# Optimization experiments

Measured on AMD Instinct MI355X. Metric: run time of the kernel, lower is better.

## Reference

```python
import jax, jax.numpy as jnp
import numpy as np
import math

B, T, C = 1, 2048, 2048
H, KVH = 32, 8
D = C // H  # 64
EPS = 1e-5
ROPE_THETA = 10000.0


def rmsnorm(x, w):
    # RMSNorm over last axis (head_dim), matches flax RMSNorm applied per-head
    var = jnp.mean(jnp.square(x), axis=-1, keepdims=True)
    return x * jax.lax.rsqrt(var + EPS) * w


def apply_rope(x, cos, sin):
    # x: [B, T, h, D]; cos/sin: [T, D//2]
    xr = x.reshape(*x.shape[:-1], D // 2, 2)
    x0, x1 = xr[..., 0], xr[..., 1]
    c = cos.reshape(1, T, 1, D // 2)
    s = sin.reshape(1, T, 1, D // 2)
    o0 = x0 * c - x1 * s
    o1 = x0 * s + x1 * c
    return jnp.stack([o0, o1], axis=-1).reshape(x.shape)


def setup_inputs() -> dict:
    key = jax.random.key(0)
    ks = jax.random.split(key, 12)
    x = jax.random.normal(ks[0], (B, T, C), jnp.float32)
    # RoPE tables
    inv_freq = 1.0 / (ROPE_THETA ** (np.arange(0, D, 2, dtype=np.float32) / D))
    angles = np.arange(T, dtype=np.float32)[:, None] * inv_freq[None, :]  # [T, D//2]
    freqs_cos = jnp.asarray(np.cos(angles))
    freqs_sin = jnp.asarray(np.sin(angles))
    # causal additive mask [1,1,T,T]
    causal = np.triu(np.full((T, T), -1e9, dtype=np.float32), k=1)
    mask = jnp.asarray(causal)[None, None]
    sc = lambda f: 1.0 / math.sqrt(f)
    return {
        "x": x,
        "freqs_cos": freqs_cos,
        "freqs_sin": freqs_sin,
        "mask": mask,
        "wq_k": jax.random.normal(ks[1], (C, H * D), jnp.float32) * sc(C),
        "wq_b": jnp.zeros((H * D,), jnp.float32),
        "wk_k": jax.random.normal(ks[2], (C, KVH * D), jnp.float32) * sc(C),
        "wk_b": jnp.zeros((KVH * D,), jnp.float32),
        "wv_k": jax.random.normal(ks[3], (C, KVH * D), jnp.float32) * sc(C),
        "wv_b": jnp.zeros((KVH * D,), jnp.float32),
        "wo_k": jax.random.normal(ks[4], (H * D, C), jnp.float32) * sc(H * D),
        "wo_b": jnp.zeros((C,), jnp.float32),
        "qn_w": jnp.ones((D,), jnp.float32),
        "kn_w": jnp.ones((D,), jnp.float32),
    }


def reference(x, freqs_cos, freqs_sin, mask, wq_k, wq_b, wk_k, wk_b, wv_k, wv_b, wo_k, wo_b, qn_w, kn_w):
    q = (x @ wq_k + wq_b).reshape(B, T, H, D)
    k = (x @ wk_k + wk_b).reshape(B, T, KVH, D)
    v = (x @ wv_k + wv_b).reshape(B, T, KVH, D)
    # QK RMSNorm over head_dim
    q = rmsnorm(q, qn_w)
    k = rmsnorm(k, kn_w)
    # RoPE
    q = apply_rope(q, freqs_cos, freqs_sin)
    k = apply_rope(k, freqs_cos, freqs_sin)
    # GQA repeat kv heads
    rep = H // KVH
    k = jnp.repeat(k, rep, axis=2)
    v = jnp.repeat(v, rep, axis=2)
    # [B, H, T, D]
    q, k, v = (jnp.swapaxes(t, 1, 2) for t in (q, k, v))
    scale = 1.0 / math.sqrt(D)
    scores = jnp.einsum("bhqd,bhkd->bhqk", q, k) * scale + mask
    attn = jax.nn.softmax(scores, axis=-1)
    out = jnp.einsum("bhqk,bhkd->bhqd", attn, v)
    out = jnp.swapaxes(out, 1, 2).reshape(B, T, H * D)
    return out @ wo_k + wo_b
```

## Files before the change

kernel.cpp:

```cpp
#include <hip/hip_runtime.h>
#include <hip/hip_bf16.h>
#include <cstdint>

typedef unsigned short u16;
typedef __attribute__((ext_vector_type(8))) short short8;
typedef __attribute__((ext_vector_type(4))) float f32x4;

__device__ __forceinline__ u16 f2bf(float f) {
  union { float f; uint32_t u; } c; c.f = f;
  return (u16)((c.u + 0x7FFFu + ((c.u >> 16) & 1u)) >> 16);
}

__device__ __forceinline__ uint32_t pack_bf16x2(float a, float b) {
  union { __hip_bfloat162 h; uint32_t u; } c;
  c.h = __float22bfloat162_rn(make_float2(a, b));
  return c.u;
}

__global__ __launch_bounds__(256) void prep_kernel(const float* __restrict__ x,
                                                   u16* __restrict__ xb,
                                                   const float* __restrict__ wq,
                                                   const float* __restrict__ wk,
                                                   const float* __restrict__ wv,
                                                   const float* __restrict__ wo,
                                                   u16* __restrict__ wqkvT,
                                                   u16* __restrict__ woT) {
  int id = blockIdx.x;
  if (id >= 2560) {
    int i = (id - 2560) * 256 + threadIdx.x;
    float4 v = ((const float4*)x)[i];
    ((ushort4*)xb)[i] = make_ushort4(f2bf(v.x), f2bf(v.y), f2bf(v.z), f2bf(v.w));
    return;
  }
  __shared__ float tile[64][65];
  const int K = 2048;
  int bx = id % 80, by = id / 80;
  const float* in; u16* out; int N, nx;
  if (bx < 32)      { in = wq; out = wqkvT;                          N = 2048; nx = bx; }
  else if (bx < 40) { in = wk; out = wqkvT + (size_t)2048 * 2048;    N = 512;  nx = bx - 32; }
  else if (bx < 48) { in = wv; out = wqkvT + (size_t)2560 * 2048;    N = 512;  nx = bx - 40; }
  else              { in = wo; out = woT;                            N = 2048; nx = bx - 48; }
  int n0 = nx * 64, k0 = by * 64;
  int t = threadIdx.x;
  int a = t & 63, b4 = t >> 6;
#pragma unroll
  for (int j = 0; j < 16; ++j) {
    int kk = j * 4 + b4;
    tile[kk][a] = in[(size_t)(k0 + kk) * N + n0 + a];
  }
  __syncthreads();
#pragma unroll
  for (int j = 0; j < 16; ++j) {
    int nn = j * 4 + b4;
    out[(size_t)(n0 + nn) * K + k0 + a] = f2bf(tile[a][nn]);
  }
}

__global__ __launch_bounds__(256, 3) void gemm_qkv(const u16* __restrict__ A,
                                                   const u16* __restrict__ Bt,
                                                   const float* __restrict__ wq_b,
                                                   const float* __restrict__ wk_b,
                                                   const float* __restrict__ wv_b,
                                                   const float* __restrict__ qn_w,
                                                   const float* __restrict__ kn_w,
                                                   const float* __restrict__ fc,
                                                   const float* __restrict__ fs,
                                                   u16* __restrict__ Qg,
                                                   u16* __restrict__ Kg,
                                                   u16* __restrict__ Vgt) {
  const int K = 2048;
  __shared__ alignas(16) u16 As[2][64 * 64];
  __shared__ alignas(16) u16 Bs[2][128 * 64];
  int nwg = gridDim.x;
  int cpx = nwg >> 3;
  int bid = blockIdx.x;
  int swz = (bid & 7) * cpx + (bid >> 3);
  int m0 = (swz & 31) << 6;
  int n0 = (swz >> 5) << 7;
  int tid = threadIdx.x;
  int w = tid >> 6, lane = tid & 63;
  int wr = w >> 1, wc = w & 1;
  int fr = lane & 15, hi = lane >> 4;
  int sw = fr & 7;

  auto STAGE = [&](int buf, int kt) {
#pragma unroll
    for (int i = 0; i < 2; ++i) {
      int chunk = i * 256 + tid;
      int row = chunk >> 3, c = chunk & 7;
      const u16* ga = A + (size_t)(m0 + row) * K + kt + ((c ^ (row & 7)) << 3);
      u16* la = &As[buf][(size_t)(i * 256 + w * 64) * 8];
      __builtin_amdgcn_global_load_lds((const __attribute__((address_space(1))) void*)ga,
                                       (__attribute__((address_space(3))) void*)la, 16, 0, 0);
    }
#pragma unroll
    for (int i = 0; i < 4; ++i) {
      int chunk = i * 256 + tid;
      int row = chunk >> 3, c = chunk & 7;
      const u16* gb = Bt + (size_t)(n0 + row) * K + kt + ((c ^ (row & 7)) << 3);
      u16* lb = &Bs[buf][(size_t)(i * 256 + w * 64) * 8];
      __builtin_amdgcn_global_load_lds((const __attribute__((address_space(1))) void*)gb,
                                       (__attribute__((address_space(3))) void*)lb, 16, 0, 0);
    }
  };

  f32x4 acc[2][4] = {};
  STAGE(0, 0);
  __syncthreads();
  int cur = 0;
  int c0 = (hi ^ sw) << 3, c1 = ((4 + hi) ^ sw) << 3;
  for (int kt = 0; kt < K; kt += 64) {
    if (kt + 64 < K) STAGE(cur ^ 1, kt + 64);
    short8 af[2][2], bf[4][2];
#pragma unroll
    for (int m = 0; m < 2; ++m) {
      int rb = (wr * 32 + m * 16 + fr) * 64;
      af[m][0] = *(const short8*)&As[cur][rb + c0];
      af[m][1] = *(const short8*)&As[cur][rb + c1];
    }
#pragma unroll
    for (int n = 0; n < 4; ++n) {
      int rb = (wc * 64 + n * 16 + fr) * 64;
      bf[n][0] = *(const short8*)&Bs[cur][rb + c0];
      bf[n][1] = *(const short8*)&Bs[cur][rb + c1];
    }
#pragma unroll
    for (int m = 0; m < 2; ++m)
#pragma unroll
      for (int n = 0; n < 4; ++n) {
        acc[m][n] = __builtin_amdgcn_mfma_f32_16x16x32_bf16(af[m][0], bf[n][0], acc[m][n], 0, 0, 0);
        acc[m][n] = __builtin_amdgcn_mfma_f32_16x16x32_bf16(af[m][1], bf[n][1], acc[m][n], 0, 0, 0);
      }
    __syncthreads();
    cur ^= 1;
  }

  int fbase = n0 + wc * 64;
  if (fbase >= 2560) {
    const float* bias = wv_b + (fbase - 2560);
    u16* vt = Vgt + (size_t)(fbase - 2560) * 2048;
    float bv[4];
#pragma unroll
    for (int n = 0; n < 4; ++n) bv[n] = bias[n * 16 + fr];
#pragma unroll
    for (int m = 0; m < 2; ++m)
#pragma unroll
      for (int r = 0; r < 4; ++r) {
        int t = m0 + wr * 32 + m * 16 + hi * 4 + r;
#pragma unroll
        for (int n = 0; n < 4; ++n)
          vt[(size_t)(n * 16 + fr) * 2048 + t] = f2bf(acc[m][n][r] + bv[n]);
      }
    return;
  }
  bool isQ = (fbase < 2048);
  const float* bias = isQ ? wq_b + fbase : wk_b + (fbase - 2048);
  const float* nw   = isQ ? qn_w : kn_w;
  float nscale      = isQ ? 0.18033688f : 1.0f;
  u16* outp = isQ ? Qg + (size_t)(fbase >> 6) * 2048 * 64
                  : Kg + (size_t)((fbase - 2048) >> 6) * 2048 * 64;
  float bv[4], nwv[4];
#pragma unroll
  for (int n = 0; n < 4; ++n) {
    bv[n] = bias[n * 16 + fr];
    nwv[n] = nw[n * 16 + fr] * nscale;
  }
#pragma unroll
  for (int m = 0; m < 2; ++m) {
#pragma unroll
    for (int r = 0; r < 4; ++r) {
      int t = m0 + wr * 32 + m * 16 + hi * 4 + r;
      float v[4];
      float sq = 0.0f;
#pragma unroll
      for (int n = 0; n < 4; ++n) { v[n] = acc[m][n][r] + bv[n]; sq += v[n] * v[n]; }
      sq += __shfl_xor(sq, 1); sq += __shfl_xor(sq, 2);
      sq += __shfl_xor(sq, 4); sq += __shfl_xor(sq, 8);
      float rr = rsqrtf(sq * (1.0f / 64.0f) + 1e-5f);
#pragma unroll
      for (int n = 0; n < 4; ++n) {
        float vn = v[n] * rr * nwv[n];
        float part = __shfl_xor(vn, 1);
        int dh = n * 16 + fr;
        float c = fc[t * 32 + (dh >> 1)];
        float s = fs[t * 32 + (dh >> 1)];
        v[n] = (dh & 1) ? (part * s + vn * c) : (vn * c - part * s);
      }
#pragma unroll
      for (int n = 0; n < 4; ++n)
        outp[(size_t)t * 64 + n * 16 + fr] = f2bf(v[n]);
    }
  }
}

__global__ __launch_bounds__(256, 4) void gemm_bt(const u16* __restrict__ A,
                                                  const u16* __restrict__ Bt,
                                                  float* __restrict__ C,
                                                  const float* __restrict__ bias,
                                                  int M, int N, int K) {
  __shared__ alignas(16) u16 As[2][64 * 64];
  __shared__ alignas(16) u16 Bs[2][64 * 64];
  int mt = M >> 6;
  int nwg = gridDim.x;
  int cpx = nwg >> 3;
  int bid = blockIdx.x;
  int swz = (bid & 7) * cpx + (bid >> 3);
  int m0 = (swz % mt) << 6;
  int n0 = (swz / mt) << 6;
  int tid = threadIdx.x;
  int w = tid >> 6, lane = tid & 63;
  int wr = w >> 1, wc = w & 1;
  int fr = lane & 15, hi = lane >> 4;
  int sw = fr & 7;

  auto STAGE = [&](int buf, int kt) {
#pragma unroll
    for (int i = 0; i < 2; ++i) {
      int chunk = i * 256 + tid;
      int row = chunk >> 3, c = chunk & 7;
      const u16* ga = A + (size_t)(m0 + row) * K + kt + ((c ^ (row & 7)) << 3);
      u16* la = &As[buf][(size_t)(i * 256 + w * 64) * 8];
      __builtin_amdgcn_global_load_lds((const __attribute__((address_space(1))) void*)ga,
                                       (__attribute__((address_space(3))) void*)la, 16, 0, 0);
      const u16* gb = Bt + (size_t)(n0 + row) * K + kt + ((c ^ (row & 7)) << 3);
      u16* lb = &Bs[buf][(size_t)(i * 256 + w * 64) * 8];
      __builtin_amdgcn_global_load_lds((const __attribute__((address_space(1))) void*)gb,
                                       (__attribute__((address_space(3))) void*)lb, 16, 0, 0);
    }
  };

  f32x4 acc[2][2] = {};
  STAGE(0, 0);
  __syncthreads();
  int cur = 0;
  int c0 = (hi ^ sw) << 3, c1 = ((4 + hi) ^ sw) << 3;
  for (int kt = 0; kt < K; kt += 64) {
    if (kt + 64 < K) STAGE(cur ^ 1, kt + 64);
    short8 af[2][2], bf[2][2];
#pragma unroll
    for (int m = 0; m < 2; ++m) {
      int rb = (wr * 32 + m * 16 + fr) * 64;
      af[m][0] = *(const short8*)&As[cur][rb + c0];
      af[m][1] = *(const short8*)&As[cur][rb + c1];
    }
#pragma unroll
    for (int n = 0; n < 2; ++n) {
      int rb = (wc * 32 + n * 16 + fr) * 64;
      bf[n][0] = *(const short8*)&Bs[cur][rb + c0];
      bf[n][1] = *(const short8*)&Bs[cur][rb + c1];
    }
#pragma unroll
    for (int m = 0; m < 2; ++m)
#pragma unroll
      for (int n = 0; n < 2; ++n) {
        acc[m][n] = __builtin_amdgcn_mfma_f32_16x16x32_bf16(af[m][0], bf[n][0], acc[m][n], 0, 0, 0);
        acc[m][n] = __builtin_amdgcn_mfma_f32_16x16x32_bf16(af[m][1], bf[n][1], acc[m][n], 0, 0, 0);
      }
    __syncthreads();
    cur ^= 1;
  }
#pragma unroll
  for (int m = 0; m < 2; ++m) {
#pragma unroll
    for (int n = 0; n < 2; ++n) {
      int gcol = n0 + wc * 32 + n * 16 + fr;
      float bvx = bias ? bias[gcol] : 0.0f;
#pragma unroll
      for (int r = 0; r < 4; ++r) {
        int grow = m0 + wr * 32 + m * 16 + hi * 4 + r;
        C[(size_t)grow * N + gcol] = acc[m][n][r] + bvx;
      }
    }
  }
}

__global__ __launch_bounds__(256, 3) void attn_kernel(const u16* __restrict__ Qg,
                                                      const u16* __restrict__ Kg,
                                                      const u16* __restrict__ Vgt,
                                                      const float* __restrict__ qn_w,
                                                      const float* __restrict__ kn_w,
                                                      u16* __restrict__ att) {
  __shared__ alignas(16) u16 Ks[2][64 * 64];
  __shared__ alignas(16) u16 Vs[2][64 * 64];
  __shared__ alignas(16) uint32_t Ps[4][16 * 36];

  int bid = blockIdx.x;
  int grp = bid >> 8, idx = bid & 255;
  int q0 = idx >> 5, h = idx & 31;
  int qt = (grp == 0) ? 31 - q0 : (grp == 1) ? 16 + q0 : (grp == 2) ? 15 - q0 : q0;
  int kvh = h >> 2;

  int tid = threadIdx.x, w = tid >> 6, lane = tid & 63;
  int fr = lane & 15, hi = lane >> 4, fk = hi * 8;

  float ba = fabsf(qn_w[lane]), bb = fabsf(kn_w[lane]);
#pragma unroll
  for (int off = 32; off >= 1; off >>= 1) {
    ba = fmaxf(ba, __shfl_xor(ba, off));
    bb = fmaxf(bb, __shfl_xor(bb, off));
  }
  float mfix = 11.5416222f * ba * bb;

  const u16* qbase = Qg + ((size_t)h * 2048 + qt * 64 + w * 16 + fr) * 64;
  short8 qf0 = *(const short8*)(qbase + fk);
  short8 qf1 = *(const short8*)(qbase + 32 + fk);
  short8 ones;
#pragma unroll
  for (int j = 0; j < 8; ++j) ones[j] = (short)0x3F80;
  f32x4 o[4] = {};
  f32x4 o_l = {};

  int row0 = tid >> 3, cc = tid & 7;
  const u16* Kbase = Kg + (size_t)kvh * 2048 * 64;
  const u16* Vtbase = Vgt + (size_t)kvh * 64 * 2048;

  short8 k0r, k1r, v0r, v1r;
  auto stage_load = [&](int kt2) {
    const u16* kb = Kbase + (size_t)kt2 * 64 * 64;
    k0r = *(const short8*)(kb + row0 * 64 + cc * 8);
    k1r = *(const short8*)(kb + (32 + row0) * 64 + cc * 8);
    const u16* vb = Vtbase + (size_t)row0 * 2048 + kt2 * 64 + cc * 8;
    v0r = *(const short8*)vb;
    v1r = *(const short8*)(vb + 32 * 2048);
  };
  auto stage_write = [&](int buf) {
    char* KsB = (char*)&Ks[buf][0];
    char* VsB = (char*)&Vs[buf][0];
    int offA = (row0 * 128 + cc * 16) ^ ((row0 & 7) << 4);
    int offB = ((32 + row0) * 128 + cc * 16) ^ ((row0 & 7) << 4);
    *(short8*)(KsB + offA) = k0r;
    *(short8*)(KsB + offB) = k1r;
    *(short8*)(VsB + offA) = v0r;
    *(short8*)(VsB + offB) = v1r;
  };

  stage_load(0);
  stage_write(0);
  __syncthreads();

  uint32_t* Pw = &Ps[w][0];
  int swzr = (fr & 7) << 4;
  int qrow = qt * 64 + w * 16 + fr;

  for (int kt = 0; kt <= qt; ++kt) {
    int buf = kt & 1;
    bool diag = (kt == qt);
    if (!diag) stage_load(kt + 1);
    const char* KsB = (const char*)&Ks[buf][0];
    const char* VsB = (const char*)&Vs[buf][0];
    f32x4 s4[4] = {};
    __builtin_amdgcn_s_setprio(1);
#pragma unroll
    for (int g = 0; g < 4; ++g) {
      int rb = (g * 16 + fr) * 128;
      short8 b0 = *(const short8*)(KsB + ((rb + hi * 16) ^ swzr));
      short8 b1 = *(const short8*)(KsB + ((rb + 64 + hi * 16) ^ swzr));
      s4[g] = __builtin_amdgcn_mfma_f32_16x16x32_bf16(b0, qf0, s4[g], 0, 0, 0);
      s4[g] = __builtin_amdgcn_mfma_f32_16x16x32_bf16(b1, qf1, s4[g], 0, 0, 0);
    }
    __builtin_amdgcn_s_setprio(0);
    if (diag) {
      int kbase = kt * 64 + hi * 4;
#pragma unroll
      for (int g = 0; g < 4; ++g)
#pragma unroll
        for (int r = 0; r < 4; ++r)
          if (kbase + g * 16 + r > qrow) s4[g][r] = -1e30f;
    }
#pragma unroll
    for (int g = 0; g < 4; ++g) {
      float p0 = exp2f(s4[g][0] - mfix);
      float p1 = exp2f(s4[g][1] - mfix);
      float p2 = exp2f(s4[g][2] - mfix);
      float p3 = exp2f(s4[g][3] - mfix);
      uint2 pk = make_uint2(pack_bf16x2(p0, p1), pack_bf16x2(p2, p3));
      *(uint2*)&Pw[fr * 36 + g * 8 + hi * 2] = pk;
    }
    asm volatile("s_waitcnt lgkmcnt(0)" ::: "memory");
    short8 pa0 = *(const short8*)&Pw[fr * 36 + hi * 4];
    short8 pa1 = *(const short8*)&Pw[fr * 36 + 16 + hi * 4];
    __builtin_amdgcn_s_setprio(1);
    o_l = __builtin_amdgcn_mfma_f32_16x16x32_bf16(pa0, ones, o_l, 0, 0, 0);
    o_l = __builtin_amdgcn_mfma_f32_16x16x32_bf16(pa1, ones, o_l, 0, 0, 0);
#pragma unroll
    for (int g2 = 0; g2 < 4; ++g2) {
      int rb = (g2 * 16 + fr) * 128;
      short8 vb0 = *(const short8*)(VsB + ((rb + hi * 16) ^ swzr));
      short8 vb1 = *(const short8*)(VsB + ((rb + 64 + hi * 16) ^ swzr));
      o[g2] = __builtin_amdgcn_mfma_f32_16x16x32_bf16(pa0, vb0, o[g2], 0, 0, 0);
      o[g2] = __builtin_amdgcn_mfma_f32_16x16x32_bf16(pa1, vb1, o[g2], 0, 0, 0);
    }
    __builtin_amdgcn_s_setprio(0);
    if (!diag) stage_write(buf ^ 1);
    __syncthreads();
  }
#pragma unroll
  for (int r = 0; r < 4; ++r) {
    float inv = 1.0f / o_l[r];
    size_t rowoff = (size_t)(qt * 64 + w * 16 + hi * 4 + r) * 2048 + h * 64;
#pragma unroll
    for (int g2 = 0; g2 < 4; ++g2)
      att[rowoff + g2 * 16 + fr] = f2bf(o[g2][r] * inv);
  }
}

extern "C" void kernel_launch(void* const* d_in, const int* in_sizes, int n_in,
                              void* d_out, int out_size, void* d_ws, size_t ws_size,
                              hipStream_t stream) {
  const float* x    = (const float*)d_in[0];
  const float* fc   = (const float*)d_in[1];
  const float* fs   = (const float*)d_in[2];
  const float* wq   = (const float*)d_in[4];
  const float* wq_b = (const float*)d_in[5];
  const float* wk   = (const float*)d_in[6];
  const float* wk_b = (const float*)d_in[7];
  const float* wv   = (const float*)d_in[8];
  const float* wv_b = (const float*)d_in[9];
  const float* wo   = (const float*)d_in[10];
  const float* wo_b = (const float*)d_in[11];
  const float* qn   = (const float*)d_in[12];
  const float* kn   = (const float*)d_in[13];
  float* out = (float*)d_out;

  char* ws = (char*)d_ws;
  u16*  xb    = (u16*)(ws);
  u16*  wqkvT = (u16*)(ws + (size_t)(8  << 20));
  u16*  woT   = (u16*)(ws + (size_t)(20 << 20));
  u16*  Qg    = (u16*)(ws + (size_t)(52 << 20));
  u16*  Kg    = (u16*)(ws + (size_t)(60 << 20));
  u16*  Vgt   = (u16*)(ws + (size_t)(62 << 20));
  u16*  att   = (u16*)(ws + (size_t)(64 << 20));

  prep_kernel<<<6656, 256, 0, stream>>>(x, xb, wq, wk, wv, wo, wqkvT, woT);
  gemm_qkv<<<32 * 24, 256, 0, stream>>>(xb, wqkvT, wq_b, wk_b, wv_b, qn, kn, fc, fs, Qg, Kg, Vgt);
  attn_kernel<<<1024, 256, 0, stream>>>(Qg, Kg, Vgt, qn, kn, att);
  gemm_bt<<<32 * 32, 256, 0, stream>>>(att, woT, out, wo_b, 2048, 2048, 2048);
}
```

Baseline: 119.6 us.

## Use 128-row query tiles with 8 waves per attention block

```diff
diff --git a/kernel.cpp b/kernel.cpp
--- a/kernel.cpp
+++ b/kernel.cpp
@@ -274,7 +274,7 @@
   }
 }
 
-__global__ __launch_bounds__(256, 3) void attn_kernel(const u16* __restrict__ Qg,
+__global__ __launch_bounds__(512, 4) void attn_kernel(const u16* __restrict__ Qg,
                                                       const u16* __restrict__ Kg,
                                                       const u16* __restrict__ Vgt,
                                                       const float* __restrict__ qn_w,
@@ -282,12 +282,12 @@
                                                       u16* __restrict__ att) {
   __shared__ alignas(16) u16 Ks[2][64 * 64];
   __shared__ alignas(16) u16 Vs[2][64 * 64];
-  __shared__ alignas(16) uint32_t Ps[4][16 * 36];
+  __shared__ alignas(16) uint32_t Ps[8][16 * 36];
 
   int bid = blockIdx.x;
   int grp = bid >> 8, idx = bid & 255;
   int q0 = idx >> 5, h = idx & 31;
-  int qt = (grp == 0) ? 31 - q0 : (grp == 1) ? 16 + q0 : (grp == 2) ? 15 - q0 : q0;
+  int p = (grp == 0) ? 15 - q0 : q0;
   int kvh = h >> 2;
 
   int tid = threadIdx.x, w = tid >> 6, lane = tid & 63;
@@ -301,7 +301,8 @@
   }
   float mfix = 11.5416222f * ba * bb;
 
-  const u16* qbase = Qg + ((size_t)h * 2048 + qt * 64 + w * 16 + fr) * 64;
+  int qrow = p * 128 + w * 16 + fr;
+  const u16* qbase = Qg + ((size_t)h * 2048 + p * 128 + w * 16 + fr) * 64;
   short8 qf0 = *(const short8*)(qbase + fk);
   short8 qf1 = *(const short8*)(qbase + 32 + fk);
   short8 ones;
@@ -314,24 +315,15 @@
   const u16* Kbase = Kg + (size_t)kvh * 2048 * 64;
   const u16* Vtbase = Vgt + (size_t)kvh * 64 * 2048;
 
-  short8 k0r, k1r, v0r, v1r;
+  short8 k0r, v0r;
   auto stage_load = [&](int kt2) {
-    const u16* kb = Kbase + (size_t)kt2 * 64 * 64;
-    k0r = *(const short8*)(kb + row0 * 64 + cc * 8);
-    k1r = *(const short8*)(kb + (32 + row0) * 64 + cc * 8);
-    const u16* vb = Vtbase + (size_t)row0 * 2048 + kt2 * 64 + cc * 8;
-    v0r = *(const short8*)vb;
-    v1r = *(const short8*)(vb + 32 * 2048);
+    k0r = *(const short8*)(Kbase + (size_t)(kt2 * 64 + row0) * 64 + cc * 8);
+    v0r = *(const short8*)(Vtbase + (size_t)row0 * 2048 + kt2 * 64 + cc * 8);
   };
   auto stage_write = [&](int buf) {
-    char* KsB = (char*)&Ks[buf][0];
-    char* VsB = (char*)&Vs[buf][0];
-    int offA = (row0 * 128 + cc * 16) ^ ((row0 & 7) << 4);
-    int offB = ((32 + row0) * 128 + cc * 16) ^ ((row0 & 7) << 4);
-    *(short8*)(KsB + offA) = k0r;
-    *(short8*)(KsB + offB) = k1r;
-    *(short8*)(VsB + offA) = v0r;
-    *(short8*)(VsB + offB) = v1r;
+    int off = (row0 * 128 + cc * 16) ^ ((row0 & 7) << 4);
+    *(short8*)((char*)&Ks[buf][0] + off) = k0r;
+    *(short8*)((char*)&Vs[buf][0] + off) = v0r;
   };
 
   stage_load(0);
@@ -340,64 +332,68 @@
 
   uint32_t* Pw = &Ps[w][0];
   int swzr = (fr & 7) << 4;
-  int qrow = qt * 64 + w * 16 + fr;
-
-  for (int kt = 0; kt <= qt; ++kt) {
+  int kmax = 2 * p + (w >> 2);
+  int nkt = 2 * p + 2;
+
+  for (int kt = 0; kt < nkt; ++kt) {
     int buf = kt & 1;
-    bool diag = (kt == qt);
-    if (!diag) stage_load(kt + 1);
-    const char* KsB = (const char*)&Ks[buf][0];
-    const char* VsB = (const char*)&Vs[buf][0];
-    f32x4 s4[4] = {};
-    __builtin_amdgcn_s_setprio(1);
-#pragma unroll
-    for (int g = 0; g < 4; ++g) {
-      int rb = (g * 16 + fr) * 128;
-      short8 b0 = *(const short8*)(KsB + ((rb + hi * 16) ^ swzr));
-      short8 b1 = *(const short8*)(KsB + ((rb + 64 + hi * 16) ^ swzr));
-      s4[g] = __builtin_amdgcn_mfma_f32_16x16x32_bf16(b0, qf0, s4[g], 0, 0, 0);
-      s4[g] = __builtin_amdgcn_mfma_f32_16x16x32_bf16(b1, qf1, s4[g], 0, 0, 0);
-    }
-    __builtin_amdgcn_s_setprio(0);
-    if (diag) {
-      int kbase = kt * 64 + hi * 4;
-#pragma unroll
-      for (int g = 0; g < 4; ++g)
-#pragma unroll
-        for (int r = 0; r < 4; ++r)
-          if (kbase + g * 16 + r > qrow) s4[g][r] = -1e30f;
-    }
-#pragma unroll
-    for (int g = 0; g < 4; ++g) {
-      float p0 = exp2f(s4[g][0] - mfix);
-      float p1 = exp2f(s4[g][1] - mfix);
-      float p2 = exp2f(s4[g][2] - mfix);
-      float p3 = exp2f(s4[g][3] - mfix);
-      uint2 pk = make_uint2(pack_bf16x2(p0, p1), pack_bf16x2(p2, p3));
-      *(uint2*)&Pw[fr * 36 + g * 8 + hi * 2] = pk;
-    }
-    asm volatile("s_waitcnt lgkmcnt(0)" ::: "memory");
-    short8 pa0 = *(const short8*)&Pw[fr * 36 + hi * 4];
-    short8 pa1 = *(const short8*)&Pw[fr * 36 + 16 + hi * 4];
-    __builtin_amdgcn_s_setprio(1);
-    o_l = __builtin_amdgcn_mfma_f32_16x16x32_bf16(pa0, ones, o_l, 0, 0, 0);
-    o_l = __builtin_amdgcn_mfma_f32_16x16x32_bf16(pa1, ones, o_l, 0, 0, 0);
-#pragma unroll
-    for (int g2 = 0; g2 < 4; ++g2) {
-      int rb = (g2 * 16 + fr) * 128;
-      short8 vb0 = *(const short8*)(VsB + ((rb + hi * 16) ^ swzr));
-      short8 vb1 = *(const short8*)(VsB + ((rb + 64 + hi * 16) ^ swzr));
-      o[g2] = __builtin_amdgcn_mfma_f32_16x16x32_bf16(pa0, vb0, o[g2], 0, 0, 0);
-      o[g2] = __builtin_amdgcn_mfma_f32_16x16x32_bf16(pa1, vb1, o[g2], 0, 0, 0);
-    }
-    __builtin_amdgcn_s_setprio(0);
-    if (!diag) stage_write(buf ^ 1);
+    bool lastIter = (kt == nkt - 1);
+    if (!lastIter) stage_load(kt + 1);
+    if (kt <= kmax) {
+      bool diag = (kt == kmax);
+      const char* KsB = (const char*)&Ks[buf][0];
+      const char* VsB = (const char*)&Vs[buf][0];
+      f32x4 s4[4] = {};
+      __builtin_amdgcn_s_setprio(1);
+#pragma unroll
+      for (int g = 0; g < 4; ++g) {
+        int rb = (g * 16 + fr) * 128;
+        short8 b0 = *(const short8*)(KsB + ((rb + hi * 16) ^ swzr));
+        short8 b1 = *(const short8*)(KsB + ((rb + 64 + hi * 16) ^ swzr));
+        s4[g] = __builtin_amdgcn_mfma_f32_16x16x32_bf16(b0, qf0, s4[g], 0, 0, 0);
+        s4[g] = __builtin_amdgcn_mfma_f32_16x16x32_bf16(b1, qf1, s4[g], 0, 0, 0);
+      }
+      __builtin_amdgcn_s_setprio(0);
+      if (diag) {
+        int kbase = kt * 64 + hi * 4;
+#pragma unroll
+        for (int g = 0; g < 4; ++g)
+#pragma unroll
+          for (int r = 0; r < 4; ++r)
+            if (kbase + g * 16 + r > qrow) s4[g][r] = -1e30f;
+      }
+#pragma unroll
+      for (int g = 0; g < 4; ++g) {
+        float p0 = exp2f(s4[g][0] - mfix);
+        float p1 = exp2f(s4[g][1] - mfix);
+        float p2 = exp2f(s4[g][2] - mfix);
+        float p3 = exp2f(s4[g][3] - mfix);
+        uint2 pk = make_uint2(pack_bf16x2(p0, p1), pack_bf16x2(p2, p3));
+        *(uint2*)&Pw[fr * 36 + g * 8 + hi * 2] = pk;
+      }
+      asm volatile("s_waitcnt lgkmcnt(0)" ::: "memory");
+      short8 pa0 = *(const short8*)&Pw[fr * 36 + hi * 4];
+      short8 pa1 = *(const short8*)&Pw[fr * 36 + 16 + hi * 4];
+      __builtin_amdgcn_s_setprio(1);
+      o_l = __builtin_amdgcn_mfma_f32_16x16x32_bf16(pa0, ones, o_l, 0, 0, 0);
+      o_l = __builtin_amdgcn_mfma_f32_16x16x32_bf16(pa1, ones, o_l, 0, 0, 0);
+#pragma unroll
+      for (int g2 = 0; g2 < 4; ++g2) {
+        int rb = (g2 * 16 + fr) * 128;
+        short8 vb0 = *(const short8*)(VsB + ((rb + hi * 16) ^ swzr));
+        short8 vb1 = *(const short8*)(VsB + ((rb + 64 + hi * 16) ^ swzr));
+        o[g2] = __builtin_amdgcn_mfma_f32_16x16x32_bf16(pa0, vb0, o[g2], 0, 0, 0);
+        o[g2] = __builtin_amdgcn_mfma_f32_16x16x32_bf16(pa1, vb1, o[g2], 0, 0, 0);
+      }
+      __builtin_amdgcn_s_setprio(0);
+    }
+    if (!lastIter) stage_write(buf ^ 1);
     __syncthreads();
   }
 #pragma unroll
   for (int r = 0; r < 4; ++r) {
     float inv = 1.0f / o_l[r];
-    size_t rowoff = (size_t)(qt * 64 + w * 16 + hi * 4 + r) * 2048 + h * 64;
+    size_t rowoff = (size_t)(p * 128 + w * 16 + hi * 4 + r) * 2048 + h * 64;
 #pragma unroll
     for (int g2 = 0; g2 < 4; ++g2)
       att[rowoff + g2 * 16 + fr] = f2bf(o[g2][r] * inv);
@@ -433,6 +429,6 @@
 
   prep_kernel<<<6656, 256, 0, stream>>>(x, xb, wq, wk, wv, wo, wqkvT, woT);
   gemm_qkv<<<32 * 24, 256, 0, stream>>>(xb, wqkvT, wq_b, wk_b, wv_b, qn, kn, fc, fs, Qg, Kg, Vgt);
-  attn_kernel<<<1024, 256, 0, stream>>>(Qg, Kg, Vgt, qn, kn, att);
+  attn_kernel<<<512, 512, 0, stream>>>(Qg, Kg, Vgt, qn, kn, att);
   gemm_bt<<<32 * 32, 256, 0, stream>>>(att, woT, out, wo_b, 2048, 2048, 2048);
 }
```

New measurement: 122.2 us. 2.2% more time.
